# Performance work log

Measured on AMD Instinct MI355X. Metric: run time of the kernel, lower is better.

## Reference

```python
import jax, jax.numpy as jnp
import numpy as np

DIM = 1024
NUM_HEADS = 16
DIM_PROJ = int(2 / 3 * 4 * DIM // 8 * 8)  # 2728, per source
EPS = 1e-5


def rms_norm(x, g):
    # NOTE: source computes sqrt(mean(x^2)) then divides by (rms + eps)
    rms = jnp.sqrt(jnp.mean(x * x, axis=-1, keepdims=True))
    return x / (rms + EPS) * g


def alibi_slopes(num_heads):
    base = (2.0 ** 8) ** (1.0 / num_heads)
    return jnp.asarray([1.0 / base ** (i + 1) for i in range(num_heads)], dtype=jnp.float32)


def setup_inputs() -> dict:
    key = jax.random.key(0)
    ks = jax.random.split(key, 7)
    B, T, C, P = 2, 2048, DIM, DIM_PROJ
    s = 0.02
    return {
        "x": jax.random.normal(ks[0], (B, T, C), dtype=jnp.float32),
        "g1": jnp.ones((C,), dtype=jnp.float32),
        "w_qkv": jax.random.normal(ks[1], (C, 3 * C), dtype=jnp.float32) * s,
        "w_o": jax.random.normal(ks[2], (C, C), dtype=jnp.float32) * s,
        "g2": jnp.ones((C,), dtype=jnp.float32),
        "W": jax.random.normal(ks[3], (C, P), dtype=jnp.float32) * s,
        "V": jax.random.normal(ks[4], (C, P), dtype=jnp.float32) * s,
        "W2": jax.random.normal(ks[5], (P, C), dtype=jnp.float32) * s,
    }


def reference(x, g1, w_qkv, w_o, g2, W, V, W2):
    B, T, C = x.shape
    H = NUM_HEADS
    Dh = C // H

    # --- attention sublayer ---
    h = rms_norm(x, g1)
    qkv = h @ w_qkv                              # [B,T,3C]
    q, k, v = jnp.split(qkv, 3, axis=-1)
    q = q.reshape(B, T, H, Dh).transpose(0, 2, 1, 3)  # [B,H,T,Dh]
    k = k.reshape(B, T, H, Dh).transpose(0, 2, 1, 3)
    v = v.reshape(B, T, H, Dh).transpose(0, 2, 1, 3)

    wei = jnp.einsum('bhqd,bhkd->bhqk', q, k)
    pos = jnp.arange(T)
    rel = (pos[None, :] - pos[:, None]).astype(jnp.float32)  # [T,T]
    m = alibi_slopes(H)[:, None, None]                        # [H,1,1]
    scale = C ** 0.5                                          # sqrt(dim), per source
    scores = wei / scale + m * rel
    causal = pos[None, :] <= pos[:, None]                     # [T,T]
    scores = jnp.where(causal[None, None], scores, -jnp.inf)
    attn = jax.nn.softmax(scores, axis=-1)

    out = jnp.einsum('bhqk,bhkd->bhqd', attn, v)
    concat = out.transpose(0, 2, 1, 3).reshape(B, T, C)
    x = concat @ w_o + x

    # --- SwiGLU sublayer ---
    h = rms_norm(x, g2)
    gated = jax.nn.silu(h @ W) * (h @ V)
    return gated @ W2 + x
```

## Files before the change

kernel.cpp:

```cpp
#include <hip/hip_runtime.h>
#include <math.h>

typedef __attribute__((ext_vector_type(8))) short bf16x8;
typedef __attribute__((ext_vector_type(4))) float f32x4;
typedef __attribute__((ext_vector_type(16))) float f32x16;

static __device__ __forceinline__ short f2bf(float x){
  union { float f; unsigned u; } a; a.f = x;
  unsigned r = a.u + 0x7fffu + ((a.u >> 16) & 1u);
  return (short)(r >> 16);
}

static __device__ __forceinline__ unsigned cvtpk(float lo, float hi){
  unsigned r; asm("v_cvt_pk_bf16_f32 %0, %1, %2" : "=v"(r) : "v"(lo), "v"(hi)); return r;
}

__global__ __launch_bounds__(256) void transpose_bf16_kernel(
    const float* __restrict__ in, short* __restrict__ out,
    int IR, int IC, int OR, int OC)
{
  __shared__ float tile[32][33];
  int i0 = blockIdx.x * 32;
  int j0 = blockIdx.y * 32;
  int tx = threadIdx.x, ty = threadIdx.y;
  #pragma unroll
  for (int r = 0; r < 32; r += 8){
    int j = j0 + ty + r, i = i0 + tx;
    tile[ty + r][tx] = (j < IR && i < IC) ? in[(size_t)j * IC + i] : 0.f;
  }
  __syncthreads();
  #pragma unroll
  for (int r = 0; r < 32; r += 8){
    int oi = i0 + ty + r, oj = j0 + tx;
    if (oi < OR && oj < OC) out[(size_t)oi * OC + oj] = f2bf(tile[tx][ty + r]);
  }
}

__global__ __launch_bounds__(256) void transpose_bb_kernel(
    const short* __restrict__ in, short* __restrict__ out)
{
  __shared__ short tile[32][33];
  int bh = blockIdx.z;
  int t0 = blockIdx.x * 32;
  int d0 = blockIdx.y * 32;
  int tx = threadIdx.x, ty = threadIdx.y;
  const short* src = in + ((size_t)bh * 2048 + t0) * 64 + d0;
  #pragma unroll
  for (int r = 0; r < 32; r += 8)
    tile[ty + r][tx] = src[(size_t)(ty + r) * 64 + tx];
  __syncthreads();
  short* dst = out + ((size_t)bh * 64 + d0) * 2048 + t0;
  #pragma unroll
  for (int r = 0; r < 32; r += 8)
    dst[(size_t)(ty + r) * 2048 + tx] = tile[tx][ty + r];
}

__global__ __launch_bounds__(256) void rmsnorm_kernel(
    const float* __restrict__ x, const float* __restrict__ g, short* __restrict__ out)
{
  int row = blockIdx.x, tid = threadIdx.x;
  const float4* xr = (const float4*)(x + (size_t)row * 1024);
  float4 v = xr[tid];
  float ss = v.x*v.x + v.y*v.y + v.z*v.z + v.w*v.w;
  #pragma unroll
  for (int m = 1; m < 64; m <<= 1) ss += __shfl_xor(ss, m, 64);
  __shared__ float sm[4];
  if ((tid & 63) == 0) sm[tid >> 6] = ss;
  __syncthreads();
  float tot = sm[0] + sm[1] + sm[2] + sm[3];
  float inv = 1.f / (sqrtf(tot * (1.f/1024.f)) + 1e-5f);
  float4 gv = ((const float4*)g)[tid];
  short4 o;
  o.x = f2bf(v.x * inv * gv.x);
  o.y = f2bf(v.y * inv * gv.y);
  o.z = f2bf(v.z * inv * gv.z);
  o.w = f2bf(v.w * inv * gv.w);
  *(short4*)(out + (size_t)row * 1024 + tid * 4) = o;
}

enum { EPI_F32 = 0, EPI_RESID = 1, EPI_QKV = 2, EPI_GATED = 3 };

template<int BM, int BN>
static __device__ __forceinline__ void dp_issue(
    const short* __restrict__ A, const short* __restrict__ Bt,
    short* __restrict__ lbuf, int K, int m0, int n0, int k0,
    int wave, int lane, int l)
{
  int g = (l * 8 + wave) * 64 + lane;
  const short* src;
  if (g < BM * 8){
    int row = g >> 3, cc = g & 7;
    src = A + (size_t)(m0 + row) * K + k0 + ((cc ^ (row & 7)) << 3);
  } else {
    int gb = g - BM * 8;
    int row = gb >> 3, cc = gb & 7;
    src = Bt + (size_t)(n0 + row) * K + k0 + ((cc ^ (row & 7)) << 3);
  }
  __builtin_amdgcn_global_load_lds((const __attribute__((address_space(1))) void*)src,
                                   (__attribute__((address_space(3))) void*)(lbuf + (size_t)g * 8),
                                   16, 0, 0);
}

template<int BM, int BN, int EPI>
__global__ __launch_bounds__(512, 2) void gemm_dp_kernel(
    const short* __restrict__ A, const short* __restrict__ Bt,
    int M, int N, int K,
    float* __restrict__ outF, short* __restrict__ outB,
    const float* __restrict__ resid, const float* __restrict__ Gprev,
    short* __restrict__ qb, short* __restrict__ kb, short* __restrict__ vb)
{
  constexpr int L  = (BM + BN) / 64;
  constexpr int WM = BM / 2, WN = BN / 4;
  constexpr int FR = WM / 16, FC = WN / 16;
  __shared__ short lds[2][(BM + BN) * 64];
  const int tid = threadIdx.x, lane = tid & 63, wave = tid >> 6;
  const int wr = wave >> 2, wc = wave & 3;
  const int la = lane & 15, lg = lane >> 4;

  int nbn = N / BN;
  int nwg = (M / BM) * nbn;
  int bid = blockIdx.x;
  int wg = ((nwg & 7) == 0) ? ((bid & 7) * (nwg >> 3) + (bid >> 3)) : bid;
  int m0 = (wg / nbn) * BM, n0 = (wg % nbn) * BN;

  f32x4 acc[FR][FC];
  #pragma unroll
  for (int i = 0; i < FR; ++i)
    #pragma unroll
    for (int j = 0; j < FC; ++j) acc[i][j] = f32x4{0.f, 0.f, 0.f, 0.f};

  const int NT = K >> 6;

  #pragma unroll
  for (int l = 0; l < L; ++l) dp_issue<BM, BN>(A, Bt, lds[0], K, m0, n0, 0,  wave, lane, l);
  #pragma unroll
  for (int l = 0; l < L; ++l) dp_issue<BM, BN>(A, Bt, lds[1], K, m0, n0, 64, wave, lane, l);

  for (int t = 0; t < NT; ++t){
    short* curb = lds[t & 1];
    if (t + 1 < NT){
      if constexpr (L == 8)      asm volatile("s_waitcnt vmcnt(8)" ::: "memory");
      else if constexpr (L == 6) asm volatile("s_waitcnt vmcnt(6)" ::: "memory");
      else                       asm volatile("s_waitcnt vmcnt(4)" ::: "memory");
    } else {
      asm volatile("s_waitcnt vmcnt(0)" ::: "memory");
    }
    __builtin_amdgcn_s_barrier();
    __builtin_amdgcn_sched_barrier(0);

    #pragma unroll
    for (int qr = 0; qr < FR / 4; ++qr){
      #pragma unroll
      for (int qc = 0; qc < FC / 2; ++qc){
        bf16x8 af[4][2], bfv[2][2];
        #pragma unroll
        for (int ii = 0; ii < 4; ++ii){
          int r = wr * WM + (qr * 4 + ii) * 16 + la;
          #pragma unroll
          for (int ks = 0; ks < 2; ++ks)
            af[ii][ks] = *(const bf16x8*)(curb + r * 64 + (((ks * 4 + lg) ^ (r & 7)) << 3));
        }
        #pragma unroll
        for (int jc = 0; jc < 2; ++jc){
          int rb = wc * WN + (qc * 2 + jc) * 16 + la;
          #pragma unroll
          for (int ks = 0; ks < 2; ++ks)
            bfv[jc][ks] = *(const bf16x8*)(curb + BM * 64 + rb * 64 + (((ks * 4 + lg) ^ (rb & 7)) << 3));
        }
        __builtin_amdgcn_s_setprio(1);
        #pragma unroll
        for (int ii = 0; ii < 4; ++ii)
          #pragma unroll
          for (int jc = 0; jc < 2; ++jc){
            acc[qr*4+ii][qc*2+jc] = __builtin_amdgcn_mfma_f32_16x16x32_bf16(
                af[ii][0], bfv[jc][0], acc[qr*4+ii][qc*2+jc], 0, 0, 0);
            acc[qr*4+ii][qc*2+jc] = __builtin_amdgcn_mfma_f32_16x16x32_bf16(
                af[ii][1], bfv[jc][1], acc[qr*4+ii][qc*2+jc], 0, 0, 0);
          }
        __builtin_amdgcn_s_setprio(0);
      }
    }
    __builtin_amdgcn_sched_barrier(0);
    __builtin_amdgcn_s_barrier();
    __builtin_amdgcn_sched_barrier(0);
    if (t + 2 < NT){
      #pragma unroll
      for (int l = 0; l < L; ++l)
        dp_issue<BM, BN>(A, Bt, curb, K, m0, n0, (t + 2) << 6, wave, lane, l);
    }
  }

  #pragma unroll
  for (int i = 0; i < FR; ++i){
    #pragma unroll
    for (int j = 0; j < FC; ++j){
      #pragma unroll
      for (int rr = 0; rr < 4; ++rr){
        int row = m0 + wr * WM + i * 16 + lg * 4 + rr;
        int col = n0 + wc * WN + j * 16 + la;
        float v = acc[i][j][rr];
        size_t idx = (size_t)row * N + col;
        if (EPI == EPI_F32){
          outF[idx] = v;
        } else if (EPI == EPI_RESID){
          outF[idx] = v + resid[idx];
        } else if (EPI == EPI_GATED){
          float gg = Gprev[idx];
          float s = gg / (1.f + __expf(-gg));
          outB[idx] = f2bf(s * v);
        } else {
          int which = col >> 10;
          int hh = (col & 1023) >> 6;
          int d = col & 63;
          int bb = row >> 11, tt = row & 2047;
          size_t o = (((size_t)(bb * 16 + hh) * 2048) + tt) * 64 + d;
          if (which == 0)      qb[o] = f2bf(v * 0.045084220f);
          else if (which == 1) kb[o] = f2bf(v);
          else                 vb[o] = f2bf(v);
        }
      }
    }
  }
}


#define KVLOAD(KF, VF, T_)                                                      \
  do {                                                                          \
    _Pragma("unroll")                                                           \
    for (int ks = 0; ks < 4; ++ks)                                              \
      KF[ks] = *(const bf16x8*)(Kg + ((size_t)((T_) * 32 + q32)) * 64 + ks * 16 + hi * 8); \
    _Pragma("unroll")                                                           \
    for (int dk = 0; dk < 4; ++dk)                                              \
      VF[dk] = *(const bf16x8*)(Vt + ((size_t)((dk >> 1) * 32 + q32)) * 2048 + (T_) * 32 + (dk & 1) * 16 + hi * 8); \
  } while (0)

#define CBASE(r) ((float)(((r) & 3) + 8 * ((r) >> 2)))
#define CBI(r)   ((((r) & 3) + 8 * ((r) >> 2)))

#define PROC(CK, CV, T_, DOPF, NK, NV)                                          \
  do {                                                                          \
    f32x16 sS;                                                                  \
    _Pragma("unroll") for (int i = 0; i < 16; ++i) sS[i] = 0.f;                 \
    sS = __builtin_amdgcn_mfma_f32_32x32x16_bf16(CK[0], qf[0], sS, 0, 0, 0);    \
    sS = __builtin_amdgcn_mfma_f32_32x32x16_bf16(CK[1], qf[1], sS, 0, 0, 0);    \
    sS = __builtin_amdgcn_mfma_f32_32x32x16_bf16(CK[2], qf[2], sS, 0, 0, 0);    \
    sS = __builtin_amdgcn_mfma_f32_32x32x16_bf16(CK[3], qf[3], sS, 0, 0, 0);    \
    if (DOPF) KVLOAD(NK, NV, (T_) + 1);                                         \
    float bb = slope2 * (float)((T_) * 32 + 4 * hi - qpos);                     \
    float sc[16];                                                               \
    _Pragma("unroll")                                                           \
    for (int r = 0; r < 16; ++r) sc[r] = (sS[r] + bb) + slope2 * CBASE(r);      \
    if ((T_) == j){                                                             \
      _Pragma("unroll")                                                         \
      for (int r = 0; r < 16; ++r)                                              \
        sc[r] = (CBI(r) + 4 * hi <= q32) ? sc[r] : -1e30f;                      \
    }                                                                           \
    float t8[8], t4[4];                                                         \
    _Pragma("unroll") for (int i = 0; i < 8; ++i) t8[i] = fmaxf(sc[i], sc[i + 8]); \
    _Pragma("unroll") for (int i = 0; i < 4; ++i) t4[i] = fmaxf(t8[i], t8[i + 4]); \
    float mx = fmaxf(fmaxf(t4[0], t4[1]), fmaxf(t4[2], t4[3]));                 \
    mx = fmaxf(mx, __shfl_xor(mx, 32, 64));                                     \
    if (!__all(mx <= m_run + 8.f)){                                             \
      float mnew = fmaxf(m_run, mx);                                            \
      float aL = exp2f(m_run - mnew);                                           \
      l_run *= aL;                                                              \
      m_run = mnew;                                                             \
      _Pragma("unroll")                                                         \
      for (int r = 0; r < 16; ++r){                                             \
        float aq = __shfl(aL, CBI(r) + 4 * hi, 64);                             \
        o0[r] *= aq; o1[r] *= aq;                                               \
      }                                                                         \
    }                                                                           \
    float pr[16];                                                               \
    _Pragma("unroll")                                                           \
    for (int r = 0; r < 16; ++r) pr[r] = exp2f(sc[r] - m_run);                  \
    _Pragma("unroll") for (int i = 0; i < 8; ++i) t8[i] = pr[i] + pr[i + 8];    \
    _Pragma("unroll") for (int i = 0; i < 4; ++i) t4[i] = t8[i] + t8[i + 4];    \
    float ps = (t4[0] + t4[1]) + (t4[2] + t4[3]);                               \
    ps += __shfl_xor(ps, 32, 64);                                               \
    l_run += ps;                                                                \
    unsigned c0 = cvtpk(pr[0], pr[1]),   c1 = cvtpk(pr[2], pr[3]);              \
    unsigned c2 = cvtpk(pr[4], pr[5]),   c3 = cvtpk(pr[6], pr[7]);              \
    unsigned c4 = cvtpk(pr[8], pr[9]),   c5 = cvtpk(pr[10], pr[11]);            \
    unsigned c6 = cvtpk(pr[12], pr[13]), c7 = cvtpk(pr[14], pr[15]);            \
    unsigned x0 = (unsigned)__shfl_xor((int)c0, 32, 64), x1 = (unsigned)__shfl_xor((int)c1, 32, 64); \
    unsigned x2 = (unsigned)__shfl_xor((int)c2, 32, 64), x3 = (unsigned)__shfl_xor((int)c3, 32, 64); \
    unsigned x4 = (unsigned)__shfl_xor((int)c4, 32, 64), x5 = (unsigned)__shfl_xor((int)c5, 32, 64); \
    unsigned x6 = (unsigned)__shfl_xor((int)c6, 32, 64), x7 = (unsigned)__shfl_xor((int)c7, 32, 64); \
    union { unsigned u[4]; bf16x8 v; } pa0u, pa1u;                              \
    pa0u.u[0] = hi ? x2 : c0;  pa0u.u[1] = hi ? x3 : c1;                        \
    pa0u.u[2] = hi ? c2 : x0;  pa0u.u[3] = hi ? c3 : x1;                        \
    pa1u.u[0] = hi ? x6 : c4;  pa1u.u[1] = hi ? x7 : c5;                        \
    pa1u.u[2] = hi ? c6 : x4;  pa1u.u[3] = hi ? c7 : x5;                        \
    o0 = __builtin_amdgcn_mfma_f32_32x32x16_bf16(pa0u.v, CV[0], o0, 0, 0, 0);   \
    o0 = __builtin_amdgcn_mfma_f32_32x32x16_bf16(pa1u.v, CV[1], o0, 0, 0, 0);   \
    o1 = __builtin_amdgcn_mfma_f32_32x32x16_bf16(pa0u.v, CV[2], o1, 0, 0, 0);   \
    o1 = __builtin_amdgcn_mfma_f32_32x32x16_bf16(pa1u.v, CV[3], o1, 0, 0, 0);   \
  } while (0)

__global__ __launch_bounds__(256) void attn_kernel(
    const short* __restrict__ qb, const short* __restrict__ kb,
    const short* __restrict__ vtb, short* __restrict__ concat)
{
  const int T = 2048;
  int id = blockIdx.x;
  int grp = id & 7;
  int j   = 63 - (id >> 3);
  int wave = threadIdx.x >> 6;
  int bh = grp * 4 + wave;
  int lane = threadIdx.x & 63;
  int q32 = lane & 31;
  int hi  = lane >> 5;
  int h = bh & 15, b = bh >> 4;

  const short* Q  = qb  + (size_t)bh * T * 64;
  const short* Kg = kb  + (size_t)bh * T * 64;
  const short* Vt = vtb + (size_t)bh * 64 * T;

  float slope2 = exp2f(-0.5f * (float)(h + 1)) * 1.44269504f;

  int q0 = j * 32;
  int qpos = q0 + q32;
  int nt = j + 1;

  bf16x8 qf[4];
  #pragma unroll
  for (int ks = 0; ks < 4; ++ks)
    qf[ks] = *(const bf16x8*)(Q + (size_t)qpos * 64 + ks * 16 + hi * 8);

  f32x16 o0, o1;
  #pragma unroll
  for (int i = 0; i < 16; ++i){ o0[i] = 0.f; o1[i] = 0.f; }
  float m_run = -1e30f, l_run = 0.f;

  bf16x8 kA[4], vA[4], kB[4], vB[4];
  KVLOAD(kA, vA, 0);

  int t = 0;
  while (1){
    PROC(kA, vA, t, (t + 1 < nt), kB, vB);
    ++t; if (t >= nt) break;
    PROC(kB, vB, t, (t + 1 < nt), kA, vA);
    ++t; if (t >= nt) break;
  }

  float linv = 1.f / l_run;
  #pragma unroll
  for (int r = 0; r < 16; ++r){
    int crow = CBI(r) + 4 * hi;
    float lq = __shfl(linv, crow, 64);
    size_t base = ((size_t)(b * 2048 + q0 + crow)) * 1024 + h * 64;
    concat[base + q32]      = f2bf(o0[r] * lq);
    concat[base + 32 + q32] = f2bf(o1[r] * lq);
  }
}

extern "C" void kernel_launch(void* const* d_in, const int* in_sizes, int n_in,
                              void* d_out, int out_size, void* d_ws, size_t ws_size,
                              hipStream_t stream)
{
  (void)in_sizes; (void)n_in; (void)out_size; (void)ws_size;
  const float* x     = (const float*)d_in[0];
  const float* g1    = (const float*)d_in[1];
  const float* w_qkv = (const float*)d_in[2];
  const float* w_o   = (const float*)d_in[3];
  const float* g2    = (const float*)d_in[4];
  const float* W     = (const float*)d_in[5];
  const float* V     = (const float*)d_in[6];
  const float* W2    = (const float*)d_in[7];
  float* out = (float*)d_out;

  char* wsb = (char*)d_ws;
  size_t off = 0;
  auto alloc = [&](size_t bytes) -> void* {
    void* p = wsb + off;
    off += (bytes + 255) & ~(size_t)255;
    return p;
  };
  short* wqkvT = (short*)alloc((size_t)3072 * 1024 * 2);
  short* woT   = (short*)alloc((size_t)1024 * 1024 * 2);
  short* WT    = (short*)alloc((size_t)2816 * 1024 * 2);
  short* VT    = (short*)alloc((size_t)2816 * 1024 * 2);
  short* W2T   = (short*)alloc((size_t)1024 * 2816 * 2);
  short* h1    = (short*)alloc((size_t)4096 * 1024 * 2);
  short* qbuf  = (short*)alloc((size_t)4096 * 1024 * 2);
  short* kbuf  = (short*)alloc((size_t)4096 * 1024 * 2);
  short* vbuf  = (short*)alloc((size_t)4096 * 1024 * 2);
  short* vtbuf = (short*)alloc((size_t)4096 * 1024 * 2);
  short* conc  = (short*)alloc((size_t)4096 * 1024 * 2);
  float* x2    = (float*)alloc((size_t)4096 * 1024 * 4);
  short* h2    = (short*)alloc((size_t)4096 * 1024 * 2);
  float* G     = (float*)alloc((size_t)4096 * 2816 * 4);
  short* gated = (short*)alloc((size_t)4096 * 2816 * 2);

  dim3 tb(32, 8);
  hipLaunchKernelGGL(transpose_bf16_kernel, dim3(96, 32), tb, 0, stream, w_qkv, wqkvT, 1024, 3072, 3072, 1024);
  hipLaunchKernelGGL(transpose_bf16_kernel, dim3(32, 32), tb, 0, stream, w_o,   woT,   1024, 1024, 1024, 1024);
  hipLaunchKernelGGL(transpose_bf16_kernel, dim3(88, 32), tb, 0, stream, W,     WT,    1024, 2728, 2816, 1024);
  hipLaunchKernelGGL(transpose_bf16_kernel, dim3(88, 32), tb, 0, stream, V,     VT,    1024, 2728, 2816, 1024);
  hipLaunchKernelGGL(transpose_bf16_kernel, dim3(32, 88), tb, 0, stream, W2,    W2T,   2728, 1024, 1024, 2816);

  hipLaunchKernelGGL(rmsnorm_kernel, dim3(4096), dim3(256), 0, stream, x, g1, h1);

  hipLaunchKernelGGL((gemm_dp_kernel<256, 128, EPI_QKV>), dim3(384), dim3(512), 0, stream,
                     h1, wqkvT, 4096, 3072, 1024,
                     (float*)nullptr, (short*)nullptr, (const float*)nullptr, (const float*)nullptr,
                     qbuf, kbuf, vbuf);

  hipLaunchKernelGGL(transpose_bb_kernel, dim3(64, 2, 32), tb, 0, stream, vbuf, vtbuf);

  hipLaunchKernelGGL(attn_kernel, dim3(512), dim3(256), 0, stream, qbuf, kbuf, vtbuf, conc);

  hipLaunchKernelGGL((gemm_dp_kernel<128, 128, EPI_RESID>), dim3(256), dim3(512), 0, stream,
                     conc, woT, 4096, 1024, 1024,
                     x2, (short*)nullptr, x, (const float*)nullptr,
                     (short*)nullptr, (short*)nullptr, (short*)nullptr);

  hipLaunchKernelGGL(rmsnorm_kernel, dim3(4096), dim3(256), 0, stream, x2, g2, h2);

  hipLaunchKernelGGL((gemm_dp_kernel<256, 128, EPI_F32>), dim3(352), dim3(512), 0, stream,
                     h2, WT, 4096, 2816, 1024,
                     G, (short*)nullptr, (const float*)nullptr, (const float*)nullptr,
                     (short*)nullptr, (short*)nullptr, (short*)nullptr);

  hipLaunchKernelGGL((gemm_dp_kernel<256, 128, EPI_GATED>), dim3(352), dim3(512), 0, stream,
                     h2, VT, 4096, 2816, 1024,
                     (float*)nullptr, gated, (const float*)nullptr, G,
                     (short*)nullptr, (short*)nullptr, (short*)nullptr);

  hipLaunchKernelGGL((gemm_dp_kernel<128, 128, EPI_RESID>), dim3(256), dim3(512), 0, stream,
                     gated, W2T, 4096, 1024, 2816,
                     out, (short*)nullptr, x2, (const float*)nullptr,
                     (short*)nullptr, (short*)nullptr, (short*)nullptr);
}
```

Before: 302.1 us.

## Process two heads per wave in attention to interleave independent softmax chains

```diff
diff --git a/kernel.cpp b/kernel.cpp
--- a/kernel.cpp
+++ b/kernel.cpp
@@ -224,32 +224,31 @@
 }
 
 
-#define KVLOAD(KF, VF, T_)                                                      \
+#define CBASE(r) ((float)(((r) & 3) + 8 * ((r) >> 2)))
+#define CBI(r)   ((((r) & 3) + 8 * ((r) >> 2)))
+
+#define KVLOAD2(S, T_)                                                          \
   do {                                                                          \
     _Pragma("unroll")                                                           \
     for (int ks = 0; ks < 4; ++ks)                                              \
-      KF[ks] = *(const bf16x8*)(Kg + ((size_t)((T_) * 32 + q32)) * 64 + ks * 16 + hi * 8); \
+      k##S[ks] = *(const bf16x8*)(Kg##S + ((size_t)((T_) * 32 + q32)) * 64 + ks * 16 + hi * 8); \
     _Pragma("unroll")                                                           \
     for (int dk = 0; dk < 4; ++dk)                                              \
-      VF[dk] = *(const bf16x8*)(Vt + ((size_t)((dk >> 1) * 32 + q32)) * 2048 + (T_) * 32 + (dk & 1) * 16 + hi * 8); \
+      v##S[dk] = *(const bf16x8*)(Vt##S + ((size_t)((dk >> 1) * 32 + q32)) * 2048 + (T_) * 32 + (dk & 1) * 16 + hi * 8); \
   } while (0)
 
-#define CBASE(r) ((float)(((r) & 3) + 8 * ((r) >> 2)))
-#define CBI(r)   ((((r) & 3) + 8 * ((r) >> 2)))
-
-#define PROC(CK, CV, T_, DOPF, NK, NV)                                          \
+#define PROC2(S, T_)                                                            \
   do {                                                                          \
     f32x16 sS;                                                                  \
     _Pragma("unroll") for (int i = 0; i < 16; ++i) sS[i] = 0.f;                 \
-    sS = __builtin_amdgcn_mfma_f32_32x32x16_bf16(CK[0], qf[0], sS, 0, 0, 0);    \
-    sS = __builtin_amdgcn_mfma_f32_32x32x16_bf16(CK[1], qf[1], sS, 0, 0, 0);    \
-    sS = __builtin_amdgcn_mfma_f32_32x32x16_bf16(CK[2], qf[2], sS, 0, 0, 0);    \
-    sS = __builtin_amdgcn_mfma_f32_32x32x16_bf16(CK[3], qf[3], sS, 0, 0, 0);    \
-    if (DOPF) KVLOAD(NK, NV, (T_) + 1);                                         \
-    float bb = slope2 * (float)((T_) * 32 + 4 * hi - qpos);                     \
+    sS = __builtin_amdgcn_mfma_f32_32x32x16_bf16(k##S[0], qf##S[0], sS, 0, 0, 0); \
+    sS = __builtin_amdgcn_mfma_f32_32x32x16_bf16(k##S[1], qf##S[1], sS, 0, 0, 0); \
+    sS = __builtin_amdgcn_mfma_f32_32x32x16_bf16(k##S[2], qf##S[2], sS, 0, 0, 0); \
+    sS = __builtin_amdgcn_mfma_f32_32x32x16_bf16(k##S[3], qf##S[3], sS, 0, 0, 0); \
+    float bb = slope##S * (float)((T_) * 32 + 4 * hi - qpos);                   \
     float sc[16];                                                               \
     _Pragma("unroll")                                                           \
-    for (int r = 0; r < 16; ++r) sc[r] = (sS[r] + bb) + slope2 * CBASE(r);      \
+    for (int r = 0; r < 16; ++r) sc[r] = (sS[r] + bb) + slope##S * CBASE(r);    \
     if ((T_) == j){                                                             \
       _Pragma("unroll")                                                         \
       for (int r = 0; r < 16; ++r)                                              \
@@ -260,25 +259,25 @@
     _Pragma("unroll") for (int i = 0; i < 4; ++i) t4[i] = fmaxf(t8[i], t8[i + 4]); \
     float mx = fmaxf(fmaxf(t4[0], t4[1]), fmaxf(t4[2], t4[3]));                 \
     mx = fmaxf(mx, __shfl_xor(mx, 32, 64));                                     \
-    if (!__all(mx <= m_run + 8.f)){                                             \
-      float mnew = fmaxf(m_run, mx);                                            \
-      float aL = exp2f(m_run - mnew);                                           \
-      l_run *= aL;                                                              \
-      m_run = mnew;                                                             \
+    if (!__all(mx <= m##S + 8.f)){                                              \
+      float mnew = fmaxf(m##S, mx);                                             \
+      float aL = exp2f(m##S - mnew);                                            \
+      l##S *= aL;                                                               \
+      m##S = mnew;                                                              \
       _Pragma("unroll")                                                         \
       for (int r = 0; r < 16; ++r){                                             \
         float aq = __shfl(aL, CBI(r) + 4 * hi, 64);                             \
-        o0[r] *= aq; o1[r] *= aq;                                               \
+        o0##S[r] *= aq; o1##S[r] *= aq;                                         \
       }                                                                         \
     }                                                                           \
     float pr[16];                                                               \
     _Pragma("unroll")                                                           \
-    for (int r = 0; r < 16; ++r) pr[r] = exp2f(sc[r] - m_run);                  \
+    for (int r = 0; r < 16; ++r) pr[r] = exp2f(sc[r] - m##S);                   \
     _Pragma("unroll") for (int i = 0; i < 8; ++i) t8[i] = pr[i] + pr[i + 8];    \
     _Pragma("unroll") for (int i = 0; i < 4; ++i) t4[i] = t8[i] + t8[i + 4];    \
     float ps = (t4[0] + t4[1]) + (t4[2] + t4[3]);                               \
     ps += __shfl_xor(ps, 32, 64);                                               \
-    l_run += ps;                                                                \
+    l##S += ps;                                                                 \
     unsigned c0 = cvtpk(pr[0], pr[1]),   c1 = cvtpk(pr[2], pr[3]);              \
     unsigned c2 = cvtpk(pr[4], pr[5]),   c3 = cvtpk(pr[6], pr[7]);              \
     unsigned c4 = cvtpk(pr[8], pr[9]),   c5 = cvtpk(pr[10], pr[11]);            \
@@ -292,10 +291,10 @@
     pa0u.u[2] = hi ? c2 : x0;  pa0u.u[3] = hi ? c3 : x1;                        \
     pa1u.u[0] = hi ? x6 : c4;  pa1u.u[1] = hi ? x7 : c5;                        \
     pa1u.u[2] = hi ? c6 : x4;  pa1u.u[3] = hi ? c7 : x5;                        \
-    o0 = __builtin_amdgcn_mfma_f32_32x32x16_bf16(pa0u.v, CV[0], o0, 0, 0, 0);   \
-    o0 = __builtin_amdgcn_mfma_f32_32x32x16_bf16(pa1u.v, CV[1], o0, 0, 0, 0);   \
-    o1 = __builtin_amdgcn_mfma_f32_32x32x16_bf16(pa0u.v, CV[2], o1, 0, 0, 0);   \
-    o1 = __builtin_amdgcn_mfma_f32_32x32x16_bf16(pa1u.v, CV[3], o1, 0, 0, 0);   \
+    o0##S = __builtin_amdgcn_mfma_f32_32x32x16_bf16(pa0u.v, v##S[0], o0##S, 0, 0, 0); \
+    o0##S = __builtin_amdgcn_mfma_f32_32x32x16_bf16(pa1u.v, v##S[1], o0##S, 0, 0, 0); \
+    o1##S = __builtin_amdgcn_mfma_f32_32x32x16_bf16(pa0u.v, v##S[2], o1##S, 0, 0, 0); \
+    o1##S = __builtin_amdgcn_mfma_f32_32x32x16_bf16(pa1u.v, v##S[3], o1##S, 0, 0, 0); \
   } while (0)
 
 __global__ __launch_bounds__(256) void attn_kernel(
@@ -304,54 +303,66 @@
 {
   const int T = 2048;
   int id = blockIdx.x;
-  int grp = id & 7;
-  int j   = 63 - (id >> 3);
+  int j  = 63 - (id >> 2);
   int wave = threadIdx.x >> 6;
-  int bh = grp * 4 + wave;
+  int u = (id & 3) * 4 + wave;
+  int bhA = 2 * u, bhB = 2 * u + 1;
   int lane = threadIdx.x & 63;
   int q32 = lane & 31;
   int hi  = lane >> 5;
-  int h = bh & 15, b = bh >> 4;
-
-  const short* Q  = qb  + (size_t)bh * T * 64;
-  const short* Kg = kb  + (size_t)bh * T * 64;
-  const short* Vt = vtb + (size_t)bh * 64 * T;
-
-  float slope2 = exp2f(-0.5f * (float)(h + 1)) * 1.44269504f;
+  int hA = bhA & 15, bA = bhA >> 4;
+  int hB = bhB & 15, bB = bhB >> 4;
+
+  const short* QA  = qb  + (size_t)bhA * T * 64;
+  const short* KgA = kb  + (size_t)bhA * T * 64;
+  const short* VtA = vtb + (size_t)bhA * 64 * T;
+  const short* QB  = qb  + (size_t)bhB * T * 64;
+  const short* KgB = kb  + (size_t)bhB * T * 64;
+  const short* VtB = vtb + (size_t)bhB * 64 * T;
+
+  float slopeA = exp2f(-0.5f * (float)(hA + 1)) * 1.44269504f;
+  float slopeB = exp2f(-0.5f * (float)(hB + 1)) * 1.44269504f;
 
   int q0 = j * 32;
   int qpos = q0 + q32;
-  int nt = j + 1;
-
-  bf16x8 qf[4];
-  #pragma unroll
-  for (int ks = 0; ks < 4; ++ks)
-    qf[ks] = *(const bf16x8*)(Q + (size_t)qpos * 64 + ks * 16 + hi * 8);
-
-  f32x16 o0, o1;
-  #pragma unroll
-  for (int i = 0; i < 16; ++i){ o0[i] = 0.f; o1[i] = 0.f; }
-  float m_run = -1e30f, l_run = 0.f;
+
+  bf16x8 qfA[4], qfB[4];
+  #pragma unroll
+  for (int ks = 0; ks < 4; ++ks){
+    qfA[ks] = *(const bf16x8*)(QA + (size_t)qpos * 64 + ks * 16 + hi * 8);
+    qfB[ks] = *(const bf16x8*)(QB + (size_t)qpos * 64 + ks * 16 + hi * 8);
+  }
+
+  f32x16 o0A, o1A, o0B, o1B;
+  #pragma unroll
+  for (int i = 0; i < 16; ++i){ o0A[i] = 0.f; o1A[i] = 0.f; o0B[i] = 0.f; o1B[i] = 0.f; }
+  float mA = -1e30f, lA = 0.f;
+  float mB = -1e30f, lB = 0.f;
 
   bf16x8 kA[4], vA[4], kB[4], vB[4];
-  KVLOAD(kA, vA, 0);
-
-  int t = 0;
-  while (1){
-    PROC(kA, vA, t, (t + 1 < nt), kB, vB);
-    ++t; if (t >= nt) break;
-    PROC(kB, vB, t, (t + 1 < nt), kA, vA);
-    ++t; if (t >= nt) break;
-  }
-
-  float linv = 1.f / l_run;
+  KVLOAD2(A, j);
+  KVLOAD2(B, j);
+
+  for (int t = j; ; --t){
+    PROC2(A, t);
+    if (t > 0) KVLOAD2(A, t - 1);
+    PROC2(B, t);
+    if (t > 0) KVLOAD2(B, t - 1);
+    if (t == 0) break;
+  }
+
+  float linvA = 1.f / lA, linvB = 1.f / lB;
   #pragma unroll
   for (int r = 0; r < 16; ++r){
     int crow = CBI(r) + 4 * hi;
-    float lq = __shfl(linv, crow, 64);
-    size_t base = ((size_t)(b * 2048 + q0 + crow)) * 1024 + h * 64;
-    concat[base + q32]      = f2bf(o0[r] * lq);
-    concat[base + 32 + q32] = f2bf(o1[r] * lq);
+    float lqA = __shfl(linvA, crow, 64);
+    float lqB = __shfl(linvB, crow, 64);
+    size_t baseA = ((size_t)(bA * 2048 + q0 + crow)) * 1024 + hA * 64;
+    size_t baseB = ((size_t)(bB * 2048 + q0 + crow)) * 1024 + hB * 64;
+    concat[baseA + q32]      = f2bf(o0A[r] * lqA);
+    concat[baseA + 32 + q32] = f2bf(o1A[r] * lqA);
+    concat[baseB + q32]      = f2bf(o0B[r] * lqB);
+    concat[baseB + 32 + q32] = f2bf(o1B[r] * lqB);
   }
 }
 
@@ -409,7 +420,7 @@
 
   hipLaunchKernelGGL(transpose_bb_kernel, dim3(64, 2, 32), tb, 0, stream, vbuf, vtbuf);
 
-  hipLaunchKernelGGL(attn_kernel, dim3(512), dim3(256), 0, stream, qbuf, kbuf, vtbuf, conc);
+  hipLaunchKernelGGL(attn_kernel, dim3(256), dim3(256), 0, stream, qbuf, kbuf, vtbuf, conc);
 
   hipLaunchKernelGGL((gemm_dp_kernel<128, 128, EPI_RESID>), dim3(256), dim3(512), 0, stream,
                      conc, woT, 4096, 1024, 1024,
```

Result: slower. 351.0 us (+16.2%).

## Split attention KV loop across two waves and pair causal query tiles per block

Applied to the files above, without the earlier changes.

```diff
diff --git a/kernel.cpp b/kernel.cpp
--- a/kernel.cpp
+++ b/kernel.cpp
@@ -224,6 +224,9 @@
 }
 
 
+#define CBASE(r) ((float)(((r) & 3) + 8 * ((r) >> 2)))
+#define CBI(r)   ((((r) & 3) + 8 * ((r) >> 2)))
+
 #define KVLOAD(KF, VF, T_)                                                      \
   do {                                                                          \
     _Pragma("unroll")                                                           \
@@ -234,9 +237,6 @@
       VF[dk] = *(const bf16x8*)(Vt + ((size_t)((dk >> 1) * 32 + q32)) * 2048 + (T_) * 32 + (dk & 1) * 16 + hi * 8); \
   } while (0)
 
-#define CBASE(r) ((float)(((r) & 3) + 8 * ((r) >> 2)))
-#define CBI(r)   ((((r) & 3) + 8 * ((r) >> 2)))
-
 #define PROC(CK, CV, T_, DOPF, NK, NV)                                          \
   do {                                                                          \
     f32x16 sS;                                                                  \
@@ -245,11 +245,11 @@
     sS = __builtin_amdgcn_mfma_f32_32x32x16_bf16(CK[1], qf[1], sS, 0, 0, 0);    \
     sS = __builtin_amdgcn_mfma_f32_32x32x16_bf16(CK[2], qf[2], sS, 0, 0, 0);    \
     sS = __builtin_amdgcn_mfma_f32_32x32x16_bf16(CK[3], qf[3], sS, 0, 0, 0);    \
-    if (DOPF) KVLOAD(NK, NV, (T_) + 1);                                         \
-    float bb = slope2 * (float)((T_) * 32 + 4 * hi - qpos);                     \
+    if (DOPF) KVLOAD(NK, NV, (T_) + 2);                                         \
+    float bb2 = slope2 * (float)((T_) * 32 + 4 * hi - qpos);                    \
     float sc[16];                                                               \
     _Pragma("unroll")                                                           \
-    for (int r = 0; r < 16; ++r) sc[r] = (sS[r] + bb) + slope2 * CBASE(r);      \
+    for (int r = 0; r < 16; ++r) sc[r] = (sS[r] + bb2) + slope2 * CBASE(r);     \
     if ((T_) == j){                                                             \
       _Pragma("unroll")                                                         \
       for (int r = 0; r < 16; ++r)                                              \
@@ -298,60 +298,94 @@
     o1 = __builtin_amdgcn_mfma_f32_32x32x16_bf16(pa1u.v, CV[3], o1, 0, 0, 0);   \
   } while (0)
 
-__global__ __launch_bounds__(256) void attn_kernel(
+__global__ __launch_bounds__(512) void attn_kernel(
     const short* __restrict__ qb, const short* __restrict__ kb,
     const short* __restrict__ vtb, short* __restrict__ concat)
 {
   const int T = 2048;
   int id = blockIdx.x;
   int grp = id & 7;
-  int j   = 63 - (id >> 3);
-  int wave = threadIdx.x >> 6;
-  int bh = grp * 4 + wave;
+  int p   = id >> 3;
+  int wid = threadIdx.x >> 6;
+  int e   = wid & 3;
+  int s   = wid >> 2;
+  int bh = grp * 4 + e;
   int lane = threadIdx.x & 63;
   int q32 = lane & 31;
   int hi  = lane >> 5;
   int h = bh & 15, b = bh >> 4;
 
+  __shared__ float partLDS[4][16][64][2];
+  __shared__ float mlLDS[4][64][2];
+
   const short* Q  = qb  + (size_t)bh * T * 64;
   const short* Kg = kb  + (size_t)bh * T * 64;
   const short* Vt = vtb + (size_t)bh * 64 * T;
 
   float slope2 = exp2f(-0.5f * (float)(h + 1)) * 1.44269504f;
 
-  int q0 = j * 32;
-  int qpos = q0 + q32;
-  int nt = j + 1;
-
-  bf16x8 qf[4];
-  #pragma unroll
-  for (int ks = 0; ks < 4; ++ks)
-    qf[ks] = *(const bf16x8*)(Q + (size_t)qpos * 64 + ks * 16 + hi * 8);
-
-  f32x16 o0, o1;
-  #pragma unroll
-  for (int i = 0; i < 16; ++i){ o0[i] = 0.f; o1[i] = 0.f; }
-  float m_run = -1e30f, l_run = 0.f;
-
-  bf16x8 kA[4], vA[4], kB[4], vB[4];
-  KVLOAD(kA, vA, 0);
-
-  int t = 0;
-  while (1){
-    PROC(kA, vA, t, (t + 1 < nt), kB, vB);
-    ++t; if (t >= nt) break;
-    PROC(kB, vB, t, (t + 1 < nt), kA, vA);
-    ++t; if (t >= nt) break;
-  }
-
-  float linv = 1.f / l_run;
-  #pragma unroll
-  for (int r = 0; r < 16; ++r){
-    int crow = CBI(r) + 4 * hi;
-    float lq = __shfl(linv, crow, 64);
-    size_t base = ((size_t)(b * 2048 + q0 + crow)) * 1024 + h * 64;
-    concat[base + q32]      = f2bf(o0[r] * lq);
-    concat[base + 32 + q32] = f2bf(o1[r] * lq);
+  for (int task = 0; task < 2; ++task){
+    int j = task ? (63 - p) : p;
+    int q0 = j * 32;
+    int qpos = q0 + q32;
+
+    bf16x8 qf[4];
+    #pragma unroll
+    for (int ks = 0; ks < 4; ++ks)
+      qf[ks] = *(const bf16x8*)(Q + (size_t)qpos * 64 + ks * 16 + hi * 8);
+
+    f32x16 o0, o1;
+    #pragma unroll
+    for (int i = 0; i < 16; ++i){ o0[i] = 0.f; o1[i] = 0.f; }
+    float m_run = -1e30f, l_run = 0.f;
+
+    if (s <= j){
+      bf16x8 kA[4], vA[4], kB[4], vB[4];
+      KVLOAD(kA, vA, s);
+      int t = s;
+      while (1){
+        PROC(kA, vA, t, (t + 2 <= j), kB, vB);
+        t += 2; if (t > j) break;
+        PROC(kB, vB, t, (t + 2 <= j), kA, vA);
+        t += 2; if (t > j) break;
+      }
+    }
+
+    if (s == 0){
+      #pragma unroll
+      for (int r2 = 0; r2 < 8; ++r2){
+        partLDS[e][r2][lane][0]     = o0[2 * r2];
+        partLDS[e][r2][lane][1]     = o0[2 * r2 + 1];
+        partLDS[e][r2 + 8][lane][0] = o1[2 * r2];
+        partLDS[e][r2 + 8][lane][1] = o1[2 * r2 + 1];
+      }
+      mlLDS[e][lane][0] = m_run;
+      mlLDS[e][lane][1] = l_run;
+    }
+    __syncthreads();
+    if (s == 1){
+      float mE = mlLDS[e][lane][0];
+      float lE = mlLDS[e][lane][1];
+      float mS = fmaxf(mE, m_run);
+      float aE = exp2f(mE - mS);
+      float aO = exp2f(m_run - mS);
+      float lT = aE * lE + aO * l_run;
+      float linv = 1.f / lT;
+      float fE = aE * linv;
+      float fO = aO * linv;
+      #pragma unroll
+      for (int r = 0; r < 16; ++r){
+        int crow = CBI(r) + 4 * hi;
+        float fEr = __shfl(fE, crow, 64);
+        float fOr = __shfl(fO, crow, 64);
+        float oE0 = partLDS[e][r >> 1][lane][r & 1];
+        float oE1 = partLDS[e][8 + (r >> 1)][lane][r & 1];
+        size_t base = ((size_t)(b * 2048 + q0 + crow)) * 1024 + h * 64;
+        concat[base + q32]      = f2bf(fEr * oE0 + fOr * o0[r]);
+        concat[base + 32 + q32] = f2bf(fEr * oE1 + fOr * o1[r]);
+      }
+    }
+    __syncthreads();
   }
 }
 
@@ -409,7 +443,7 @@
 
   hipLaunchKernelGGL(transpose_bb_kernel, dim3(64, 2, 32), tb, 0, stream, vbuf, vtbuf);
 
-  hipLaunchKernelGGL(attn_kernel, dim3(512), dim3(256), 0, stream, qbuf, kbuf, vtbuf, conc);
+  hipLaunchKernelGGL(attn_kernel, dim3(256), dim3(512), 0, stream, qbuf, kbuf, vtbuf, conc);
 
   hipLaunchKernelGGL((gemm_dp_kernel<128, 128, EPI_RESID>), dim3(256), dim3(512), 0, stream,
                      conc, woT, 4096, 1024, 1024,
```

Measured after the change: 299.5 us. No clear change (-0.9%).
